# Kernel tuning notes

Hardware: AMD Instinct MI355X
Metric: run time of the kernel (lower is better)

The kernel has to match this reference:

```python
import jax, jax.numpy as jnp
import numpy as np

# Module hyperparameters (from __init__ defaults / init_kwargs)
A_PLUS = 0.005
A_MINUS = 0.00525
TAU_PLUS = 20.0
TAU_MINUS = 20.0
DT = 1.0

B, T, N_PRE, N_POST = 512, 100, 256, 256
SPIKE_RATE = 0.1


def setup_inputs() -> dict:
    key = jax.random.key(0)
    k1, k2, k3 = jax.random.split(key, 3)
    pre_spikes = (jax.random.uniform(k1, (B, T, N_PRE)) < SPIKE_RATE).astype(jnp.float32)
    post_spikes = (jax.random.uniform(k2, (B, T, N_POST)) < SPIKE_RATE).astype(jnp.float32)
    weights = jax.random.uniform(k3, (N_PRE, N_POST), dtype=jnp.float32)
    return {"pre_spikes": pre_spikes, "post_spikes": post_spikes, "weights": weights}


def _pre_trace(pre_tbn, decay):
    """trace[t] = sum_{tau=1..t} decay^tau * pre[t-tau]  (exact recurrence).

    pre_tbn: [T, B, N]. Returns [T, B, N] with trace[0] = 0.
    """
    def step(carry, x_t):
        # emit trace[t] = carry, then carry' = decay * (carry + pre[t])
        return decay * (carry + x_t), carry
    _, trace = jax.lax.scan(step, jnp.zeros_like(pre_tbn[0]), pre_tbn)
    return trace


def reference(pre_spikes, post_spikes, weights):
    """Classical STDP weight update.

    With T <= int(tau_plus*5) the original nested t/tau loops equal:
      dW[p,q] = (1/(B*T)) * sum_{t,b} (A+ * trace+[t,b,p] - A- * trace-[t,b,p]) * post[b,t,q]
    where trace+/- are exponential pre-synaptic eligibility traces.
    """
    batch, time_steps, _ = pre_spikes.shape
    pre_t = jnp.transpose(pre_spikes, (1, 0, 2))    # [T, B, n_pre]
    post_t = jnp.transpose(post_spikes, (1, 0, 2))  # [T, B, n_post]

    decay_plus = jnp.exp(jnp.float32(-DT / TAU_PLUS))
    decay_minus = jnp.exp(jnp.float32(-DT / TAU_MINUS))

    trace_plus = _pre_trace(pre_t, decay_plus)    # LTP: pre fires before post
    trace_minus = _pre_trace(pre_t, decay_minus)  # LTD: pre fires before post (depression of reversed pairing)

    eff = A_PLUS * trace_plus - A_MINUS * trace_minus  # [T, B, n_pre]
    weight_update = jnp.einsum('tbp,tbq->pq', eff, post_t) / (batch * time_steps)
    # original initializes update as zeros_like(weights); output shape matches weights
    return weight_update + jnp.zeros_like(weights)
```

## Files before the change

kernel.cpp:

```cpp
#include <hip/hip_runtime.h>
#include <stdint.h>

#define B_SZ   512
#define T_SZ   100
#define NPRE   256
#define NPOST  256
#define KTOT   (B_SZ * T_SZ)

typedef __bf16 bf16x8 __attribute__((ext_vector_type(8)));
typedef float  floatx4 __attribute__((ext_vector_type(4)));

__device__ __forceinline__ uint32_t bf16_rne(float v) {
    uint32_t bits = __float_as_uint(v);
    return (bits + 0x7FFFu + ((bits >> 16) & 1u)) >> 16;
}
__device__ __forceinline__ uint32_t pack_trunc2(float a, float b) {
    return (__float_as_uint(a) >> 16) | (__float_as_uint(b) & 0xFFFF0000u);
}

__global__ __launch_bounds__(256) void stdp_trace_prep(
    const float* __restrict__ pre, unsigned short* __restrict__ trace_t)
{
    __shared__ __align__(16) unsigned short T_lds[4][256][8];

    const int b = blockIdx.x;
    const int p = threadIdx.x;
    const int lane = p & 63, wave = p >> 6;
    const float decay = 0.95122942450071400910f;
    const float* src = pre + (size_t)b * (T_SZ * NPRE) + p;

    float carry = 0.0f;
    for (int kc = 0; kc < 4; ++kc) {
        uint32_t pk[16];
        if (kc < 3) {
            float x[32];
#pragma unroll
            for (int j = 0; j < 32; ++j)
                x[j] = src[(size_t)(kc * 32 + j) * NPRE];
#pragma unroll
            for (int j = 0; j < 16; ++j) {
                uint32_t lo = bf16_rne(carry);
                carry = decay * (carry + x[2 * j]);
                uint32_t hi = bf16_rne(carry);
                carry = decay * (carry + x[2 * j + 1]);
                pk[j] = lo | (hi << 16);
            }
        } else {
            float x[4];
#pragma unroll
            for (int j = 0; j < 4; ++j)
                x[j] = src[(size_t)(96 + j) * NPRE];
#pragma unroll
            for (int j = 0; j < 2; ++j) {
                uint32_t lo = bf16_rne(carry);
                carry = decay * (carry + x[2 * j]);
                uint32_t hi = bf16_rne(carry);
                carry = decay * (carry + x[2 * j + 1]);
                pk[j] = lo | (hi << 16);
            }
#pragma unroll
            for (int j = 2; j < 16; ++j) pk[j] = 0u;
        }
#pragma unroll
        for (int o = 0; o < 4; ++o)
            *(uint4*)&T_lds[o][p][0] =
                make_uint4(pk[o * 4], pk[o * 4 + 1], pk[o * 4 + 2], pk[o * 4 + 3]);
        __syncthreads();
#pragma unroll
        for (int i = 0; i < 4; ++i) {
            int pg = wave * 4 + i;
            uint4 v = *(const uint4*)&T_lds[lane >> 4][pg * 16 + (lane & 15)][0];
            *(uint4*)(trace_t + (((size_t)(b * 4 + kc) * 16 + pg) << 9) + lane * 8) = v;
        }
        __syncthreads();
    }
}

__global__ __launch_bounds__(512) void stdp_gemm(
    const unsigned short* __restrict__ trace_t,
    const float* __restrict__ post,
    float* __restrict__ partial)
{
    __shared__ __align__(16) unsigned short B_lds[64][512];

    const int bx = blockIdx.x;
    const int s  = bx & 127;
    const int pt = bx >> 7;
    const int tid = threadIdx.x;
    const int lane = tid & 63, wave = tid >> 6;
    const int wp = wave & 3, wq = wave >> 2;
    const int l15 = lane & 15, l4 = lane >> 4;

    const int q = tid & 255, hh = tid >> 8;
    const int qg = q >> 4, q15 = q & 15;

    floatx4 acc[2][8] = {};

    for (int lb = 0; lb < 4; ++lb) {
        const int b = s * 4 + lb;

        bf16x8 a_pf[4][2];
#pragma unroll
        for (int kc = 0; kc < 4; ++kc)
#pragma unroll
            for (int f = 0; f < 2; ++f) {
                int pg = pt * 8 + wp * 2 + f;
                a_pf[kc][f] = *(const bf16x8*)(
                    trace_t + (((size_t)(b * 4 + kc) * 16 + pg) << 9) + lane * 8);
            }

        const float* pb = post + (size_t)b * (T_SZ * NPOST) + q;
        if (hh == 0) {
#pragma unroll
            for (int half = 0; half < 2; ++half) {
                float x[32];
#pragma unroll
                for (int j = 0; j < 32; ++j)
                    x[j] = pb[(size_t)(half * 32 + j) * NPOST];
#pragma unroll
                for (int o = 0; o < 4; ++o) {
                    int oct = half * 4 + o;
                    uint4 v = make_uint4(pack_trunc2(x[o * 8 + 0], x[o * 8 + 1]),
                                         pack_trunc2(x[o * 8 + 2], x[o * 8 + 3]),
                                         pack_trunc2(x[o * 8 + 4], x[o * 8 + 5]),
                                         pack_trunc2(x[o * 8 + 6], x[o * 8 + 7]));
                    *(uint4*)&B_lds[(oct >> 2) * 16 + qg][(((oct & 3) * 16 + q15)) * 8] = v;
                }
            }
        } else {
            float x[32];
#pragma unroll
            for (int j = 0; j < 32; ++j)
                x[j] = pb[(size_t)(64 + j) * NPOST];
            float y[4];
#pragma unroll
            for (int j = 0; j < 4; ++j)
                y[j] = pb[(size_t)(96 + j) * NPOST];
#pragma unroll
            for (int o = 0; o < 4; ++o) {
                int oct = 8 + o;
                uint4 v = make_uint4(pack_trunc2(x[o * 8 + 0], x[o * 8 + 1]),
                                     pack_trunc2(x[o * 8 + 2], x[o * 8 + 3]),
                                     pack_trunc2(x[o * 8 + 4], x[o * 8 + 5]),
                                     pack_trunc2(x[o * 8 + 6], x[o * 8 + 7]));
                *(uint4*)&B_lds[(oct >> 2) * 16 + qg][(((oct & 3) * 16 + q15)) * 8] = v;
            }
            *(uint4*)&B_lds[3 * 16 + qg][(q15) * 8] =
                make_uint4(pack_trunc2(y[0], y[1]), pack_trunc2(y[2], y[3]), 0u, 0u);
#pragma unroll
            for (int o = 13; o < 16; ++o)
                *(uint4*)&B_lds[3 * 16 + qg][(((o & 3) * 16 + q15)) * 8] =
                    make_uint4(0u, 0u, 0u, 0u);
        }
        __syncthreads();

#pragma unroll
        for (int kc = 0; kc < 4; ++kc) {
            bf16x8 bb[8];
#pragma unroll
            for (int g = 0; g < 8; ++g)
                bb[g] = *(const bf16x8*)&B_lds[kc * 16 + wq * 8 + g][lane * 8];
#pragma unroll
            for (int f = 0; f < 2; ++f)
#pragma unroll
                for (int g = 0; g < 8; ++g)
                    acc[f][g] = __builtin_amdgcn_mfma_f32_16x16x32_bf16(
                        a_pf[kc][f], bb[g], acc[f][g], 0, 0, 0);
        }
        __syncthreads();
    }

    float* pout = partial + (size_t)bx * (128 * 256);
#pragma unroll
    for (int f = 0; f < 2; ++f) {
        int r0 = wp * 32 + f * 16 + l4 * 4;
#pragma unroll
        for (int g = 0; g < 8; ++g) {
            int c = wq * 128 + g * 16 + l15;
#pragma unroll
            for (int v = 0; v < 4; ++v)
                pout[(size_t)(r0 + v) * 256 + c] = acc[f][g][v];
        }
    }
}

__global__ __launch_bounds__(256) void stdp_reduce1(
    const float* __restrict__ partial, float* __restrict__ tmp)
{
    const int t = blockIdx.x * 256 + threadIdx.x;
    const int g = t >> 16;
    const int e = t & 65535;
    const int pt = e >> 15;
    const float* src = partial + ((size_t)(pt * 128 + g * 16)) * 32768 + (e & 32767);
    float a4[4] = {};
#pragma unroll
    for (int i = 0; i < 4; ++i)
#pragma unroll
        for (int u = 0; u < 4; ++u)
            a4[u] += src[(size_t)(u * 4 + i) * 32768];
    tmp[t] = (a4[0] + a4[1]) + (a4[2] + a4[3]);
}

__global__ __launch_bounds__(256) void stdp_reduce2(
    const float* __restrict__ tmp, float* __restrict__ out)
{
    const int idx = blockIdx.x * 256 + threadIdx.x;
    float a[4];
#pragma unroll
    for (int u = 0; u < 4; ++u)
        a[u] = tmp[(size_t)(2 * u) * 65536 + idx] +
               tmp[(size_t)(2 * u + 1) * 65536 + idx];
    const float scale = (0.005f - 0.00525f) * (1.0f / (float)KTOT);
    out[idx] = ((a[0] + a[1]) + (a[2] + a[3])) * scale;
}

extern "C" void kernel_launch(void* const* d_in, const int* in_sizes, int n_in,
                              void* d_out, int out_size, void* d_ws, size_t ws_size,
                              hipStream_t stream)
{
    const float* pre  = (const float*)d_in[0];
    const float* post = (const float*)d_in[1];
    float* out = (float*)d_out;

    unsigned short* trace_t = (unsigned short*)d_ws;
    float* partial = (float*)((char*)d_ws + (size_t)33554432);
    float* tmp     = (float*)((char*)d_ws + (size_t)67108864);

    stdp_trace_prep<<<512, 256, 0, stream>>>(pre, trace_t);
    stdp_gemm<<<256, 512, 0, stream>>>(trace_t, post, partial);
    stdp_reduce1<<<2048, 256, 0, stream>>>(partial, tmp);
    stdp_reduce2<<<256, 256, 0, stream>>>(tmp, out);
}
```

Baseline: 153.7 us.

## Fuse trace prep, GEMM and reduction into one cooperative kernel with grid syncs

Merges the four separate launches (trace prep, GEMM, two-stage reduce) into a single cooperative kernel of 256 blocks, with grid-wide syncs between the phases. Each block handles two batch traces in the prep phase. The two reduction passes collapse into one pass that sums 64 partials per thread pair and combines them with a lane shuffle. This removes launch gaps and the intermediate tmp buffer round-trip. In exchange, the reduce phase now has fewer threads doing longer serial sums, and grid.sync adds its own cost.

```diff
diff --git a/kernel.cpp b/kernel.cpp
--- a/kernel.cpp
+++ b/kernel.cpp
@@ -1,5 +1,8 @@
 #include <hip/hip_runtime.h>
+#include <hip/hip_cooperative_groups.h>
 #include <stdint.h>
+
+namespace cg = cooperative_groups;
 
 #define B_SZ   512
 #define T_SZ   100
@@ -18,200 +21,199 @@
     return (__float_as_uint(a) >> 16) | (__float_as_uint(b) & 0xFFFF0000u);
 }
 
-__global__ __launch_bounds__(256) void stdp_trace_prep(
-    const float* __restrict__ pre, unsigned short* __restrict__ trace_t)
+__global__ __launch_bounds__(512) void stdp_mega(
+    const float* __restrict__ pre, const float* __restrict__ post,
+    unsigned short* __restrict__ trace_t, float* __restrict__ partial,
+    float* __restrict__ out)
 {
-    __shared__ __align__(16) unsigned short T_lds[4][256][8];
-
-    const int b = blockIdx.x;
-    const int p = threadIdx.x;
-    const int lane = p & 63, wave = p >> 6;
-    const float decay = 0.95122942450071400910f;
-    const float* src = pre + (size_t)b * (T_SZ * NPRE) + p;
-
-    float carry = 0.0f;
-    for (int kc = 0; kc < 4; ++kc) {
-        uint32_t pk[16];
-        if (kc < 3) {
-            float x[32];
-#pragma unroll
-            for (int j = 0; j < 32; ++j)
-                x[j] = src[(size_t)(kc * 32 + j) * NPRE];
-#pragma unroll
-            for (int j = 0; j < 16; ++j) {
-                uint32_t lo = bf16_rne(carry);
-                carry = decay * (carry + x[2 * j]);
-                uint32_t hi = bf16_rne(carry);
-                carry = decay * (carry + x[2 * j + 1]);
-                pk[j] = lo | (hi << 16);
-            }
-        } else {
-            float x[4];
-#pragma unroll
-            for (int j = 0; j < 4; ++j)
-                x[j] = src[(size_t)(96 + j) * NPRE];
-#pragma unroll
-            for (int j = 0; j < 2; ++j) {
-                uint32_t lo = bf16_rne(carry);
-                carry = decay * (carry + x[2 * j]);
-                uint32_t hi = bf16_rne(carry);
-                carry = decay * (carry + x[2 * j + 1]);
-                pk[j] = lo | (hi << 16);
-            }
-#pragma unroll
-            for (int j = 2; j < 16; ++j) pk[j] = 0u;
+    __shared__ __align__(16) unsigned char smem[65536];
+    cg::grid_group grid = cg::this_grid();
+
+    const int bx  = blockIdx.x;
+    const int tid = threadIdx.x;
+
+    {
+        const int g = tid >> 8;
+        const int p = tid & 255;
+        const int lane = p & 63, wave = p >> 6;
+        const int b = 2 * bx + g;
+        unsigned short (*T_lds)[256][8] =
+            (unsigned short (*)[256][8])(smem + g * 16384);
+        const float decay = 0.95122942450071400910f;
+        const float* src = pre + (size_t)b * (T_SZ * NPRE) + p;
+
+        float carry = 0.0f;
+        for (int kc = 0; kc < 4; ++kc) {
+            uint32_t pk[16];
+            if (kc < 3) {
+                float x[32];
+#pragma unroll
+                for (int j = 0; j < 32; ++j)
+                    x[j] = src[(size_t)(kc * 32 + j) * NPRE];
+#pragma unroll
+                for (int j = 0; j < 16; ++j) {
+                    uint32_t lo = bf16_rne(carry);
+                    carry = decay * (carry + x[2 * j]);
+                    uint32_t hi = bf16_rne(carry);
+                    carry = decay * (carry + x[2 * j + 1]);
+                    pk[j] = lo | (hi << 16);
+                }
+            } else {
+                float x[4];
+#pragma unroll
+                for (int j = 0; j < 4; ++j)
+                    x[j] = src[(size_t)(96 + j) * NPRE];
+#pragma unroll
+                for (int j = 0; j < 2; ++j) {
+                    uint32_t lo = bf16_rne(carry);
+                    carry = decay * (carry + x[2 * j]);
+                    uint32_t hi = bf16_rne(carry);
+                    carry = decay * (carry + x[2 * j + 1]);
+                    pk[j] = lo | (hi << 16);
+                }
+#pragma unroll
+                for (int j = 2; j < 16; ++j) pk[j] = 0u;
+            }
+#pragma unroll
+            for (int o = 0; o < 4; ++o)
+                *(uint4*)&T_lds[o][p][0] =
+                    make_uint4(pk[o * 4], pk[o * 4 + 1], pk[o * 4 + 2], pk[o * 4 + 3]);
+            __syncthreads();
+#pragma unroll
+            for (int i = 0; i < 4; ++i) {
+                int pg = wave * 4 + i;
+                uint4 v = *(const uint4*)&T_lds[lane >> 4][pg * 16 + (lane & 15)][0];
+                *(uint4*)(trace_t + (((size_t)(b * 4 + kc) * 16 + pg) << 9) + lane * 8) = v;
+            }
+            __syncthreads();
         }
-#pragma unroll
-        for (int o = 0; o < 4; ++o)
-            *(uint4*)&T_lds[o][p][0] =
-                make_uint4(pk[o * 4], pk[o * 4 + 1], pk[o * 4 + 2], pk[o * 4 + 3]);
-        __syncthreads();
-#pragma unroll
-        for (int i = 0; i < 4; ++i) {
-            int pg = wave * 4 + i;
-            uint4 v = *(const uint4*)&T_lds[lane >> 4][pg * 16 + (lane & 15)][0];
-            *(uint4*)(trace_t + (((size_t)(b * 4 + kc) * 16 + pg) << 9) + lane * 8) = v;
-        }
-        __syncthreads();
     }
-}
-
-__global__ __launch_bounds__(512) void stdp_gemm(
-    const unsigned short* __restrict__ trace_t,
-    const float* __restrict__ post,
-    float* __restrict__ partial)
-{
-    __shared__ __align__(16) unsigned short B_lds[64][512];
-
-    const int bx = blockIdx.x;
-    const int s  = bx & 127;
-    const int pt = bx >> 7;
-    const int tid = threadIdx.x;
-    const int lane = tid & 63, wave = tid >> 6;
-    const int wp = wave & 3, wq = wave >> 2;
-    const int l15 = lane & 15, l4 = lane >> 4;
-
-    const int q = tid & 255, hh = tid >> 8;
-    const int qg = q >> 4, q15 = q & 15;
-
-    floatx4 acc[2][8] = {};
-
-    for (int lb = 0; lb < 4; ++lb) {
-        const int b = s * 4 + lb;
-
-        bf16x8 a_pf[4][2];
-#pragma unroll
-        for (int kc = 0; kc < 4; ++kc)
-#pragma unroll
-            for (int f = 0; f < 2; ++f) {
-                int pg = pt * 8 + wp * 2 + f;
-                a_pf[kc][f] = *(const bf16x8*)(
-                    trace_t + (((size_t)(b * 4 + kc) * 16 + pg) << 9) + lane * 8);
-            }
-
-        const float* pb = post + (size_t)b * (T_SZ * NPOST) + q;
-        if (hh == 0) {
-#pragma unroll
-            for (int half = 0; half < 2; ++half) {
+
+    __threadfence();
+    grid.sync();
+
+    {
+        unsigned short (*B_lds)[512] = (unsigned short (*)[512])smem;
+
+        const int s  = bx & 127;
+        const int pt = bx >> 7;
+        const int lane = tid & 63, wave = tid >> 6;
+        const int wp = wave & 3, wq = wave >> 2;
+        const int l15 = lane & 15, l4 = lane >> 4;
+        const int q = tid & 255, hh = tid >> 8;
+        const int qg = q >> 4, q15 = q & 15;
+
+        floatx4 acc[2][8] = {};
+
+        for (int lb = 0; lb < 4; ++lb) {
+            const int b = s * 4 + lb;
+
+            bf16x8 a_pf[4][2];
+#pragma unroll
+            for (int kc = 0; kc < 4; ++kc)
+#pragma unroll
+                for (int f = 0; f < 2; ++f) {
+                    int pg = pt * 8 + wp * 2 + f;
+                    a_pf[kc][f] = *(const bf16x8*)(
+                        trace_t + (((size_t)(b * 4 + kc) * 16 + pg) << 9) + lane * 8);
+                }
+
+            const float* pb = post + (size_t)b * (T_SZ * NPOST) + q;
+            if (hh == 0) {
+#pragma unroll
+                for (int half = 0; half < 2; ++half) {
+                    float x[32];
+#pragma unroll
+                    for (int j = 0; j < 32; ++j)
+                        x[j] = pb[(size_t)(half * 32 + j) * NPOST];
+#pragma unroll
+                    for (int o = 0; o < 4; ++o) {
+                        int oct = half * 4 + o;
+                        uint4 v = make_uint4(pack_trunc2(x[o * 8 + 0], x[o * 8 + 1]),
+                                             pack_trunc2(x[o * 8 + 2], x[o * 8 + 3]),
+                                             pack_trunc2(x[o * 8 + 4], x[o * 8 + 5]),
+                                             pack_trunc2(x[o * 8 + 6], x[o * 8 + 7]));
+                        *(uint4*)&B_lds[(oct >> 2) * 16 + qg][(((oct & 3) * 16 + q15)) * 8] = v;
+                    }
+                }
+            } else {
                 float x[32];
 #pragma unroll
                 for (int j = 0; j < 32; ++j)
-                    x[j] = pb[(size_t)(half * 32 + j) * NPOST];
+                    x[j] = pb[(size_t)(64 + j) * NPOST];
+                float y[4];
+#pragma unroll
+                for (int j = 0; j < 4; ++j)
+                    y[j] = pb[(size_t)(96 + j) * NPOST];
 #pragma unroll
                 for (int o = 0; o < 4; ++o) {
-                    int oct = half * 4 + o;
+                    int oct = 8 + o;
                     uint4 v = make_uint4(pack_trunc2(x[o * 8 + 0], x[o * 8 + 1]),
                                          pack_trunc2(x[o * 8 + 2], x[o * 8 + 3]),
                                          pack_trunc2(x[o * 8 + 4], x[o * 8 + 5]),
                                          pack_trunc2(x[o * 8 + 6], x[o * 8 + 7]));
                     *(uint4*)&B_lds[(oct >> 2) * 16 + qg][(((oct & 3) * 16 + q15)) * 8] = v;
                 }
-            }
-        } else {
-            float x[32];
-#pragma unroll
-            for (int j = 0; j < 32; ++j)
-                x[j] = pb[(size_t)(64 + j) * NPOST];
-            float y[4];
-#pragma unroll
-            for (int j = 0; j < 4; ++j)
-                y[j] = pb[(size_t)(96 + j) * NPOST];
-#pragma unroll
-            for (int o = 0; o < 4; ++o) {
-                int oct = 8 + o;
-                uint4 v = make_uint4(pack_trunc2(x[o * 8 + 0], x[o * 8 + 1]),
-                                     pack_trunc2(x[o * 8 + 2], x[o * 8 + 3]),
-                                     pack_trunc2(x[o * 8 + 4], x[o * 8 + 5]),
-                                     pack_trunc2(x[o * 8 + 6], x[o * 8 + 7]));
-                *(uint4*)&B_lds[(oct >> 2) * 16 + qg][(((oct & 3) * 16 + q15)) * 8] = v;
-            }
-            *(uint4*)&B_lds[3 * 16 + qg][(q15) * 8] =
-                make_uint4(pack_trunc2(y[0], y[1]), pack_trunc2(y[2], y[3]), 0u, 0u);
-#pragma unroll
-            for (int o = 13; o < 16; ++o)
-                *(uint4*)&B_lds[3 * 16 + qg][(((o & 3) * 16 + q15)) * 8] =
-                    make_uint4(0u, 0u, 0u, 0u);
+                *(uint4*)&B_lds[3 * 16 + qg][(q15) * 8] =
+                    make_uint4(pack_trunc2(y[0], y[1]), pack_trunc2(y[2], y[3]), 0u, 0u);
+#pragma unroll
+                for (int o = 13; o < 16; ++o)
+                    *(uint4*)&B_lds[3 * 16 + qg][(((o & 3) * 16 + q15)) * 8] =
+                        make_uint4(0u, 0u, 0u, 0u);
+            }
+            __syncthreads();
+
+#pragma unroll
+            for (int kc = 0; kc < 4; ++kc) {
+                bf16x8 bb[8];
+#pragma unroll
+                for (int gg = 0; gg < 8; ++gg)
+                    bb[gg] = *(const bf16x8*)&B_lds[kc * 16 + wq * 8 + gg][lane * 8];
+#pragma unroll
+                for (int f = 0; f < 2; ++f)
+#pragma unroll
+                    for (int gg = 0; gg < 8; ++gg)
+                        acc[f][gg] = __builtin_amdgcn_mfma_f32_16x16x32_bf16(
+                            a_pf[kc][f], bb[gg], acc[f][gg], 0, 0, 0);
+            }
+            __syncthreads();
         }
-        __syncthreads();
-
-#pragma unroll
-        for (int kc = 0; kc < 4; ++kc) {
-            bf16x8 bb[8];
-#pragma unroll
-            for (int g = 0; g < 8; ++g)
-                bb[g] = *(const bf16x8*)&B_lds[kc * 16 + wq * 8 + g][lane * 8];
-#pragma unroll
-            for (int f = 0; f < 2; ++f)
-#pragma unroll
-                for (int g = 0; g < 8; ++g)
-                    acc[f][g] = __builtin_amdgcn_mfma_f32_16x16x32_bf16(
-                        a_pf[kc][f], bb[g], acc[f][g], 0, 0, 0);
-        }
-        __syncthreads();
-    }
-
-    float* pout = partial + (size_t)bx * (128 * 256);
-#pragma unroll
-    for (int f = 0; f < 2; ++f) {
-        int r0 = wp * 32 + f * 16 + l4 * 4;
-#pragma unroll
-        for (int g = 0; g < 8; ++g) {
-            int c = wq * 128 + g * 16 + l15;
-#pragma unroll
-            for (int v = 0; v < 4; ++v)
-                pout[(size_t)(r0 + v) * 256 + c] = acc[f][g][v];
+
+        float* pout = partial + (size_t)bx * (128 * 256);
+#pragma unroll
+        for (int f = 0; f < 2; ++f) {
+            int r0 = wp * 32 + f * 16 + l4 * 4;
+#pragma unroll
+            for (int gg = 0; gg < 8; ++gg) {
+                int c = wq * 128 + gg * 16 + l15;
+#pragma unroll
+                for (int v = 0; v < 4; ++v)
+                    pout[(size_t)(r0 + v) * 256 + c] = acc[f][gg][v];
+            }
         }
     }
-}
-
-__global__ __launch_bounds__(256) void stdp_reduce1(
-    const float* __restrict__ partial, float* __restrict__ tmp)
-{
-    const int t = blockIdx.x * 256 + threadIdx.x;
-    const int g = t >> 16;
-    const int e = t & 65535;
-    const int pt = e >> 15;
-    const float* src = partial + ((size_t)(pt * 128 + g * 16)) * 32768 + (e & 32767);
-    float a4[4] = {};
-#pragma unroll
-    for (int i = 0; i < 4; ++i)
-#pragma unroll
-        for (int u = 0; u < 4; ++u)
-            a4[u] += src[(size_t)(u * 4 + i) * 32768];
-    tmp[t] = (a4[0] + a4[1]) + (a4[2] + a4[3]);
-}
-
-__global__ __launch_bounds__(256) void stdp_reduce2(
-    const float* __restrict__ tmp, float* __restrict__ out)
-{
-    const int idx = blockIdx.x * 256 + threadIdx.x;
-    float a[4];
-#pragma unroll
-    for (int u = 0; u < 4; ++u)
-        a[u] = tmp[(size_t)(2 * u) * 65536 + idx] +
-               tmp[(size_t)(2 * u + 1) * 65536 + idx];
-    const float scale = (0.005f - 0.00525f) * (1.0f / (float)KTOT);
-    out[idx] = ((a[0] + a[1]) + (a[2] + a[3])) * scale;
+
+    __threadfence();
+    grid.sync();
+
+    {
+        const int gid  = bx * 512 + tid;
+        const int elem = gid >> 1;
+        const int half = gid & 1;
+        const int pt = elem >> 15;
+        const int i  = elem & 32767;
+        const float* src = partial + ((size_t)(pt * 128 + half * 64)) * 32768 + i;
+        float a4[4] = {};
+#pragma unroll
+        for (int k = 0; k < 16; ++k)
+#pragma unroll
+            for (int u = 0; u < 4; ++u)
+                a4[u] += src[(size_t)(u * 16 + k) * 32768];
+        float v = (a4[0] + a4[1]) + (a4[2] + a4[3]);
+        v += __shfl_xor(v, 1, 64);
+        const float scale = (0.005f - 0.00525f) * (1.0f / (float)KTOT);
+        if (half == 0) out[elem] = v * scale;
+    }
 }
 
 extern "C" void kernel_launch(void* const* d_in, const int* in_sizes, int n_in,
@@ -224,10 +226,9 @@
 
     unsigned short* trace_t = (unsigned short*)d_ws;
     float* partial = (float*)((char*)d_ws + (size_t)33554432);
-    float* tmp     = (float*)((char*)d_ws + (size_t)67108864);
-
-    stdp_trace_prep<<<512, 256, 0, stream>>>(pre, trace_t);
-    stdp_gemm<<<256, 512, 0, stream>>>(trace_t, post, partial);
-    stdp_reduce1<<<2048, 256, 0, stream>>>(partial, tmp);
-    stdp_reduce2<<<256, 256, 0, stream>>>(tmp, out);
-}
+
+    void* args[] = {(void*)&pre, (void*)&post, (void*)&trace_t,
+                    (void*)&partial, (void*)&out};
+    hipLaunchCooperativeKernel((const void*)stdp_mega, dim3(256), dim3(512),
+                               args, 0, stream);
+}
```

Measured after the change: 341.9 us. +122.5%, slower.

## Fuse trace computation into GEMM kernel, staging traces through LDS

Applied to the files above, without the earlier changes.

Removes the separate trace-prep kernel and its bf16 trace buffer in global memory. Each GEMM block now computes the exponential pre-synaptic traces for its own 4 batches and 128 pre-neurons in registers, holding 50 packed words per thread. Each batch's traces are then written into a new LDS A tile, which the MFMA loop reads. This saves one launch and a global write plus read of the traces. In exchange it adds register pressure, more LDS, and a serial recurrence at the start of every GEMM block. Per-step trace writes are done by only a quarter of the threads.

```diff
diff --git a/kernel.cpp b/kernel.cpp
--- a/kernel.cpp
+++ b/kernel.cpp
@@ -18,69 +18,11 @@
     return (__float_as_uint(a) >> 16) | (__float_as_uint(b) & 0xFFFF0000u);
 }
 
-__global__ __launch_bounds__(256) void stdp_trace_prep(
-    const float* __restrict__ pre, unsigned short* __restrict__ trace_t)
-{
-    __shared__ __align__(16) unsigned short T_lds[4][256][8];
-
-    const int b = blockIdx.x;
-    const int p = threadIdx.x;
-    const int lane = p & 63, wave = p >> 6;
-    const float decay = 0.95122942450071400910f;
-    const float* src = pre + (size_t)b * (T_SZ * NPRE) + p;
-
-    float carry = 0.0f;
-    for (int kc = 0; kc < 4; ++kc) {
-        uint32_t pk[16];
-        if (kc < 3) {
-            float x[32];
-#pragma unroll
-            for (int j = 0; j < 32; ++j)
-                x[j] = src[(size_t)(kc * 32 + j) * NPRE];
-#pragma unroll
-            for (int j = 0; j < 16; ++j) {
-                uint32_t lo = bf16_rne(carry);
-                carry = decay * (carry + x[2 * j]);
-                uint32_t hi = bf16_rne(carry);
-                carry = decay * (carry + x[2 * j + 1]);
-                pk[j] = lo | (hi << 16);
-            }
-        } else {
-            float x[4];
-#pragma unroll
-            for (int j = 0; j < 4; ++j)
-                x[j] = src[(size_t)(96 + j) * NPRE];
-#pragma unroll
-            for (int j = 0; j < 2; ++j) {
-                uint32_t lo = bf16_rne(carry);
-                carry = decay * (carry + x[2 * j]);
-                uint32_t hi = bf16_rne(carry);
-                carry = decay * (carry + x[2 * j + 1]);
-                pk[j] = lo | (hi << 16);
-            }
-#pragma unroll
-            for (int j = 2; j < 16; ++j) pk[j] = 0u;
-        }
-#pragma unroll
-        for (int o = 0; o < 4; ++o)
-            *(uint4*)&T_lds[o][p][0] =
-                make_uint4(pk[o * 4], pk[o * 4 + 1], pk[o * 4 + 2], pk[o * 4 + 3]);
-        __syncthreads();
-#pragma unroll
-        for (int i = 0; i < 4; ++i) {
-            int pg = wave * 4 + i;
-            uint4 v = *(const uint4*)&T_lds[lane >> 4][pg * 16 + (lane & 15)][0];
-            *(uint4*)(trace_t + (((size_t)(b * 4 + kc) * 16 + pg) << 9) + lane * 8) = v;
-        }
-        __syncthreads();
-    }
-}
-
-__global__ __launch_bounds__(512) void stdp_gemm(
-    const unsigned short* __restrict__ trace_t,
-    const float* __restrict__ post,
+__global__ __launch_bounds__(512) void stdp_fused_gemm(
+    const float* __restrict__ pre, const float* __restrict__ post,
     float* __restrict__ partial)
 {
+    __shared__ __align__(16) unsigned short A_lds[32][512];
     __shared__ __align__(16) unsigned short B_lds[64][512];
 
     const int bx = blockIdx.x;
@@ -91,6 +33,42 @@
     const int wp = wave & 3, wq = wave >> 2;
     const int l15 = lane & 15, l4 = lane >> 4;
 
+    const int p_loc = tid & 127, lbo = tid >> 7;
+    uint32_t pk[50];
+    {
+        const int b = s * 4 + lbo;
+        const float decay = 0.95122942450071400910f;
+        const float* src = pre + (size_t)b * (T_SZ * NPRE) + pt * 128 + p_loc;
+        float carry = 0.0f;
+#pragma unroll
+        for (int kc = 0; kc < 3; ++kc) {
+            float x[32];
+#pragma unroll
+            for (int j = 0; j < 32; ++j)
+                x[j] = src[(size_t)(kc * 32 + j) * NPRE];
+#pragma unroll
+            for (int j = 0; j < 16; ++j) {
+                uint32_t lo = bf16_rne(carry);
+                carry = decay * (carry + x[2 * j]);
+                uint32_t hi = bf16_rne(carry);
+                carry = decay * (carry + x[2 * j + 1]);
+                pk[kc * 16 + j] = lo | (hi << 16);
+            }
+        }
+        float x[4];
+#pragma unroll
+        for (int j = 0; j < 4; ++j)
+            x[j] = src[(size_t)(96 + j) * NPRE];
+#pragma unroll
+        for (int j = 0; j < 2; ++j) {
+            uint32_t lo = bf16_rne(carry);
+            carry = decay * (carry + x[2 * j]);
+            uint32_t hi = bf16_rne(carry);
+            carry = decay * (carry + x[2 * j + 1]);
+            pk[48 + j] = lo | (hi << 16);
+        }
+    }
+
     const int q = tid & 255, hh = tid >> 8;
     const int qg = q >> 4, q15 = q & 15;
 
@@ -99,15 +77,21 @@
     for (int lb = 0; lb < 4; ++lb) {
         const int b = s * 4 + lb;
 
-        bf16x8 a_pf[4][2];
-#pragma unroll
-        for (int kc = 0; kc < 4; ++kc)
-#pragma unroll
-            for (int f = 0; f < 2; ++f) {
-                int pg = pt * 8 + wp * 2 + f;
-                a_pf[kc][f] = *(const bf16x8*)(
-                    trace_t + (((size_t)(b * 4 + kc) * 16 + pg) << 9) + lane * 8);
-            }
+        if (lbo == lb) {
+            const int pg = p_loc >> 4, lp = p_loc & 15;
+#pragma unroll
+            for (int kc = 0; kc < 3; ++kc)
+#pragma unroll
+                for (int l4w = 0; l4w < 4; ++l4w)
+                    *(uint4*)&A_lds[kc * 8 + pg][(l4w * 16 + lp) * 8] =
+                        make_uint4(pk[kc * 16 + l4w * 4], pk[kc * 16 + l4w * 4 + 1],
+                                   pk[kc * 16 + l4w * 4 + 2], pk[kc * 16 + l4w * 4 + 3]);
+            *(uint4*)&A_lds[24 + pg][lp * 8] = make_uint4(pk[48], pk[49], 0u, 0u);
+#pragma unroll
+            for (int l4w = 1; l4w < 4; ++l4w)
+                *(uint4*)&A_lds[24 + pg][(l4w * 16 + lp) * 8] =
+                    make_uint4(0u, 0u, 0u, 0u);
+        }
 
         const float* pb = post + (size_t)b * (T_SZ * NPOST) + q;
         if (hh == 0) {
@@ -156,7 +140,10 @@
 
 #pragma unroll
         for (int kc = 0; kc < 4; ++kc) {
-            bf16x8 bb[8];
+            bf16x8 a[2], bb[8];
+#pragma unroll
+            for (int f = 0; f < 2; ++f)
+                a[f] = *(const bf16x8*)&A_lds[kc * 8 + wp * 2 + f][lane * 8];
 #pragma unroll
             for (int g = 0; g < 8; ++g)
                 bb[g] = *(const bf16x8*)&B_lds[kc * 16 + wq * 8 + g][lane * 8];
@@ -165,7 +152,7 @@
 #pragma unroll
                 for (int g = 0; g < 8; ++g)
                     acc[f][g] = __builtin_amdgcn_mfma_f32_16x16x32_bf16(
-                        a_pf[kc][f], bb[g], acc[f][g], 0, 0, 0);
+                        a[f], bb[g], acc[f][g], 0, 0, 0);
         }
         __syncthreads();
     }
@@ -222,12 +209,10 @@
     const float* post = (const float*)d_in[1];
     float* out = (float*)d_out;
 
-    unsigned short* trace_t = (unsigned short*)d_ws;
-    float* partial = (float*)((char*)d_ws + (size_t)33554432);
-    float* tmp     = (float*)((char*)d_ws + (size_t)67108864);
-
-    stdp_trace_prep<<<512, 256, 0, stream>>>(pre, trace_t);
-    stdp_gemm<<<256, 512, 0, stream>>>(trace_t, post, partial);
+    float* partial = (float*)d_ws;
+    float* tmp     = (float*)((char*)d_ws + (size_t)33554432);
+
+    stdp_fused_gemm<<<256, 512, 0, stream>>>(pre, post, partial);
     stdp_reduce1<<<2048, 256, 0, stream>>>(partial, tmp);
     stdp_reduce2<<<256, 256, 0, stream>>>(tmp, out);
 }
```

After: 144.6 us. 1.06x faster.
